# Performance work log

Measured on AMD Instinct MI355X. Metric: run time of the kernel, lower is better.

The kernel has to match this reference:

```python
import jax, jax.numpy as jnp
import numpy as np

HIDDEN = 512
SCALE = 1.0 / np.sqrt(HIDDEN).astype(np.float32)
MASK_FILL = -1e20


def setup_inputs() -> dict:
    key = jax.random.key(0)
    k1, k2 = jax.random.split(key)
    B, S, D = 4, 4096, HIDDEN
    X = jax.random.normal(k1, (B, S, D), dtype=jnp.float32)
    W = jax.random.normal(k2, (D, 3 * D), dtype=jnp.float32) * (1.0 / np.sqrt(D))
    b = jnp.zeros((3 * D,), dtype=jnp.float32)
    attention_mask = jnp.ones((B, 1, S), dtype=jnp.int32)
    return {"X": X, "W": W, "b": b, "attention_mask": attention_mask}


def reference(X, W, b, attention_mask):
    # fused QKV projection: [B,S,3D]
    QKV = jnp.einsum('bsd,de->bse', X, W) + b
    Q, K, V = jnp.split(QKV, 3, axis=-1)
    # full score matrix [B,S,S] (the memory-bound part)
    scores = jnp.einsum('bqd,bkd->bqk', Q, K)
    # faithful: mask BEFORE scaling (fill value also gets divided by sqrt(d))
    scores = jnp.where(attention_mask == 0, MASK_FILL, scores)
    attn = jax.nn.softmax(scores * SCALE, axis=-1)
    # dropout disabled (eval mode) for deterministic reference
    out = jnp.einsum('bqk,bkd->bqd', attn, V)
    return out
```

## Files before the change

kernel.cpp:

```cpp
#include <hip/hip_runtime.h>
#include <cstdint>

#define B_  4
#define S_  4096
#define D_  512

#define SCALEF 0.04419417382415922f
#define QSF    0.06375885f
#define MASK_FILLF -1e20f
#define MASKQ  -6.375885e18f
#define FMAX2  17.312340f

typedef __attribute__((ext_vector_type(8))) short b16x8;
typedef __attribute__((ext_vector_type(4))) float f32x4;
typedef __attribute__((ext_vector_type(16))) float f32x16;

__device__ __forceinline__ unsigned short f2bf(float f) {
    unsigned int u = __builtin_bit_cast(unsigned int, f);
    u += 0x7fffu + ((u >> 16) & 1u);
    return (unsigned short)(u >> 16);
}

__device__ __forceinline__ float exp2fast(float x) {
#if __has_builtin(__builtin_amdgcn_exp2f)
    return __builtin_amdgcn_exp2f(x);
#else
    return __expf(x * 0.69314718056f);
#endif
}

__device__ __forceinline__ void gl_lds16(const void* gp, void* lp) {
    __builtin_amdgcn_global_load_lds(
        (const __attribute__((address_space(1))) unsigned int*)(uintptr_t)gp,
        (__attribute__((address_space(3))) unsigned int*)(uintptr_t)lp,
        16, 0, 0);
}

__global__ __launch_bounds__(256) void cast_x_kernel(const float* __restrict__ X,
                                                     unsigned short* __restrict__ Xb) {
    int i = (blockIdx.x * 256 + threadIdx.x) * 4;
    float4 v = *(const float4*)(X + i);
    ushort4 o;
    o.x = f2bf(v.x); o.y = f2bf(v.y); o.z = f2bf(v.z); o.w = f2bf(v.w);
    *(ushort4*)(Xb + i) = o;
}

__global__ __launch_bounds__(256) void cast_wt_kernel(const float* __restrict__ W,
                                                      unsigned short* __restrict__ Wt) {
    __shared__ float t[32][33];
    int tx = threadIdx.x & 31, ty0 = threadIdx.x >> 5;
    int e0 = blockIdx.x * 32;
    int d0 = blockIdx.y * 32;
#pragma unroll
    for (int p = 0; p < 4; ++p) {
        int ty = ty0 + p * 8;
        t[ty][tx] = W[(size_t)(d0 + ty) * 1536 + e0 + tx];
    }
    __syncthreads();
#pragma unroll
    for (int p = 0; p < 4; ++p) {
        int ty = ty0 + p * 8;
        Wt[(size_t)(e0 + ty) * 512 + d0 + tx] = f2bf(t[tx][ty]);
    }
}

__global__ __launch_bounds__(256) void qkv_gemm_kernel(
    const unsigned short* __restrict__ Xb, const unsigned short* __restrict__ Wt,
    const float* __restrict__ bias,
    unsigned short* __restrict__ Qb, unsigned short* __restrict__ Kb,
    unsigned short* __restrict__ Vt) {
    __shared__ char lds[32768];
    const int tid = threadIdx.x, lane = tid & 63, wave = tid >> 6;
    const int quad = lane >> 4, kcol = lane & 15;
    const int wm = wave & 1, wn = wave >> 1;
    const int row0 = blockIdx.x * 128;
    const int col0 = blockIdx.y * 128;

    unsigned agl[2], bgl[2], lloc[2];
#pragma unroll
    for (int i = 0; i < 2; ++i) {
        int L = (wave * 2 + i) * 64 + lane;
        int r = L >> 2;
        int c = (L & 3) ^ ((r >> 1) & 3);
        agl[i] = (unsigned)((row0 + r) * 1024 + c * 16);
        bgl[i] = (unsigned)((col0 + r) * 1024 + c * 16);
        lloc[i] = (unsigned)(((wave * 2 + i) * 64) * 16);
    }

    f32x4 acc[4][4];
#pragma unroll
    for (int mt = 0; mt < 4; ++mt)
#pragma unroll
        for (int nt = 0; nt < 4; ++nt) acc[mt][nt] = (f32x4){0.f, 0.f, 0.f, 0.f};

    auto stage = [&](int kk) {
        char* la = lds + (kk & 1) * 16384;
        char* lb = la + 8192;
#pragma unroll
        for (int i = 0; i < 2; ++i) {
            gl_lds16((const char*)Xb + agl[i] + kk * 64, la + lloc[i]);
            gl_lds16((const char*)Wt + bgl[i] + kk * 64, lb + lloc[i]);
        }
    };

    stage(0);
    for (int kk = 0; kk < 16; ++kk) {
        __syncthreads();
        if (kk < 15) stage(kk + 1);
        const char* la = lds + (kk & 1) * 16384;
        const char* lb = la + 8192;
        b16x8 af[4], bfr[4];
#pragma unroll
        for (int mt = 0; mt < 4; ++mt) {
            int rr = wm * 64 + mt * 16 + kcol;
            af[mt] = *(const b16x8*)(la + rr * 64 + ((quad ^ ((rr >> 1) & 3)) << 4));
        }
#pragma unroll
        for (int nt = 0; nt < 4; ++nt) {
            int rr = wn * 64 + nt * 16 + kcol;
            bfr[nt] = *(const b16x8*)(lb + rr * 64 + ((quad ^ ((rr >> 1) & 3)) << 4));
        }
#pragma unroll
        for (int mt = 0; mt < 4; ++mt)
#pragma unroll
            for (int nt = 0; nt < 4; ++nt)
                acc[mt][nt] = __builtin_amdgcn_mfma_f32_16x16x32_bf16(af[mt], bfr[nt], acc[mt][nt], 0, 0, 0);
    }

    const int colbase = col0 + wn * 64;
    const int sec = colbase >> 9;
    const int cbase = colbase & 511;
    float bv[4];
#pragma unroll
    for (int nt = 0; nt < 4; ++nt) bv[nt] = bias[colbase + nt * 16 + kcol];

    if (sec < 2) {
        unsigned short* dst = sec == 0 ? Qb : Kb;
        const float scl = sec == 0 ? QSF : 1.0f;
#pragma unroll
        for (int mt = 0; mt < 4; ++mt) {
            int rg0 = row0 + wm * 64 + mt * 16 + quad * 4;
#pragma unroll
            for (int r = 0; r < 4; ++r) {
                size_t rowoff = (size_t)(rg0 + r) * 512;
#pragma unroll
                for (int nt = 0; nt < 4; ++nt)
                    dst[rowoff + cbase + nt * 16 + kcol] = f2bf((acc[mt][nt][r] + bv[nt]) * scl);
            }
        }
    } else {
#pragma unroll
        for (int mt = 0; mt < 4; ++mt) {
            int g0 = row0 + wm * 64 + mt * 16 + quad * 4;
#pragma unroll
            for (int r = 0; r < 4; ++r) {
                int g = g0 + r;
                int s = g & 4095;
                size_t pbase = (((size_t)(g >> 12) * 128 + (s >> 5)) << 14) + (s & 31);
#pragma unroll
                for (int nt = 0; nt < 4; ++nt) {
                    int d = cbase + nt * 16 + kcol;
                    Vt[pbase + (size_t)d * 32] = f2bf(acc[mt][nt][r] + bv[nt]);
                }
            }
        }
    }
}

__global__ __launch_bounds__(384, 2) void flash_kernel(
    const unsigned short* __restrict__ Qb, const unsigned short* __restrict__ Kb,
    const unsigned short* __restrict__ Vt, const int* __restrict__ maskG,
    float* __restrict__ Out) {
    extern __shared__ char smem[];
    const int tid = threadIdx.x;
    const int lane = tid & 63;
    const int wave = tid >> 6;
    const int lin = blockIdx.x;
    const int b = lin & 3;
    const int qrow0 = (lin >> 2) * 64;
    const int NT = 128;

    char* ldsK = smem;
    unsigned short* Pb = (unsigned short*)(smem + 65536);
    float* lbuf = (float*)Pb;

    const char* kgbase = (const char*)(Kb + (size_t)b * S_ * D_);
    const char* vgbase = (const char*)Vt + (size_t)b * 128 * 32768;
    const int* mrow = maskG + b * S_;

    if (wave < 2) {
        const int keyrow = lane & 31;
        const int hh = lane >> 5;
        const int swz = lane & 7;

        b16x8 qf[32];
        {
            const unsigned short* qptr =
                Qb + (size_t)(b * S_ + qrow0 + wave * 32 + keyrow) * D_ + hh * 8;
#pragma unroll
            for (int ks = 0; ks < 32; ++ks) qf[ks] = *(const b16x8*)(qptr + ks * 16);
        }
        float lsum16[16];
#pragma unroll
        for (int r = 0; r < 16; ++r) lsum16[r] = 0.f;

        for (int t = 0; t < NT; ++t) {
            __syncthreads();
            const char* kl = ldsK + (t & 1) * 32768;
            f32x16 sA, sB;
#pragma unroll
            for (int i = 0; i < 16; ++i) { sA[i] = 0.f; sB[i] = 0.f; }
#pragma unroll
            for (int ks = 0; ks < 32; ++ks) {
                b16x8 kf = *(const b16x8*)(kl + keyrow * 1024 +
                                           (((ks * 2 + hh) ^ swz) << 4));
                if (ks & 1) sB = __builtin_amdgcn_mfma_f32_32x32x16_bf16(qf[ks], kf, sB, 0, 0, 0);
                else        sA = __builtin_amdgcn_mfma_f32_32x32x16_bf16(qf[ks], kf, sA, 0, 0, 0);
            }
            const bool um = mrow[t * 32 + keyrow] != 0;
            unsigned short* Pcur = Pb + (t & 1) * 2560;
#pragma unroll
            for (int r = 0; r < 16; ++r) {
                float sv = sA[r] + sB[r];
                float lg = um ? sv : MASKQ;
                float ex = exp2fast(lg - FMAX2);
                lsum16[r] += ex;
                int row = (r & 3) + 8 * (r >> 2) + 4 * hh + wave * 32;
                Pcur[row * 40 + keyrow] = f2bf(ex);
            }
        }
        __syncthreads();

#pragma unroll
        for (int r = 0; r < 16; ++r) {
            float l = lsum16[r];
            l += __shfl_xor(l, 1);
            l += __shfl_xor(l, 2);
            l += __shfl_xor(l, 4);
            l += __shfl_xor(l, 8);
            l += __shfl_xor(l, 16);
            if (keyrow == 0) {
                int row = (r & 3) + 8 * (r >> 2) + 4 * hh + wave * 32;
                lbuf[row] = 1.0f / l;
            }
        }
        __syncthreads();
    } else {
        const int ws = wave - 2;
        const int dw = ws * 128;
        const int quad = lane >> 4;
        const int kcol = lane & 15;

        unsigned kgl[8], kll[8];
#pragma unroll
        for (int i = 0; i < 8; ++i) {
            int r = ws * 8 + i;
            kgl[i] = (unsigned)(r * 1024 + (lane ^ i) * 16);
            kll[i] = (unsigned)(r * 1024);
        }

        f32x4 o[4][8];
#pragma unroll
        for (int m = 0; m < 4; ++m)
#pragma unroll
            for (int n = 0; n < 8; ++n) o[m][n] = (f32x4){0.f, 0.f, 0.f, 0.f};

        {
#pragma unroll
            for (int i = 0; i < 8; ++i) gl_lds16(kgbase + kgl[i], ldsK + kll[i]);
        }

        for (int t = 0; t < NT; ++t) {
            __syncthreads();

            b16x8 vf[8];
            if (t > 0) {
                const char* vtile = vgbase + (size_t)(t - 1) * 32768;
#pragma unroll
                for (int n = 0; n < 8; ++n)
                    vf[n] = *(const b16x8*)(vtile + (size_t)(dw + n * 16 + kcol) * 64 + quad * 16);
            }

            if (t + 1 < NT) {
                const char* kg = kgbase + (size_t)(t + 1) * 32768;
                char* kl2 = ldsK + ((t + 1) & 1) * 32768;
#pragma unroll
                for (int i = 0; i < 8; ++i) gl_lds16(kg + kgl[i], kl2 + kll[i]);
            }

            if (t > 0) {
                const unsigned short* Pprev = Pb + ((t - 1) & 1) * 2560;
#pragma unroll
                for (int m = 0; m < 4; ++m) {
                    b16x8 pf = *(const b16x8*)((const char*)Pprev + (m * 16 + kcol) * 80 + quad * 16);
#pragma unroll
                    for (int n = 0; n < 8; ++n)
                        o[m][n] = __builtin_amdgcn_mfma_f32_16x16x32_bf16(pf, vf[n], o[m][n], 0, 0, 0);
                }
            }
        }
        __syncthreads();

        {
            const char* vtile = vgbase + (size_t)(NT - 1) * 32768;
            b16x8 vf[8];
#pragma unroll
            for (int n = 0; n < 8; ++n)
                vf[n] = *(const b16x8*)(vtile + (size_t)(dw + n * 16 + kcol) * 64 + quad * 16);
            const unsigned short* Pprev = Pb + ((NT - 1) & 1) * 2560;
#pragma unroll
            for (int m = 0; m < 4; ++m) {
                b16x8 pf = *(const b16x8*)((const char*)Pprev + (m * 16 + kcol) * 80 + quad * 16);
#pragma unroll
                for (int n = 0; n < 8; ++n)
                    o[m][n] = __builtin_amdgcn_mfma_f32_16x16x32_bf16(pf, vf[n], o[m][n], 0, 0, 0);
            }
        }
        __syncthreads();

#pragma unroll
        for (int m = 0; m < 4; ++m) {
            f32x4 lv = *(const f32x4*)(lbuf + m * 16 + quad * 4);
#pragma unroll
            for (int r = 0; r < 4; ++r) {
                size_t off = ((size_t)b * S_ + qrow0 + m * 16 + quad * 4 + r) * D_ + dw + kcol;
#pragma unroll
                for (int n = 0; n < 8; ++n) Out[off + n * 16] = o[m][n][r] * lv[r];
            }
        }
    }
}

extern "C" void kernel_launch(void* const* d_in, const int* in_sizes, int n_in,
                              void* d_out, int out_size, void* d_ws, size_t ws_size,
                              hipStream_t stream) {
    const float* X = (const float*)d_in[0];
    const float* W = (const float*)d_in[1];
    const float* bias = (const float*)d_in[2];
    const int* mask = (const int*)d_in[3];
    float* out = (float*)d_out;

    char* w = (char*)d_ws;
    unsigned short* Xb = (unsigned short*)w;  w += (size_t)16384 * 512 * 2;
    unsigned short* Wt = (unsigned short*)w;  w += (size_t)1536 * 512 * 2;
    unsigned short* Qb = (unsigned short*)w;  w += (size_t)16384 * 512 * 2;
    unsigned short* Kb = (unsigned short*)w;  w += (size_t)16384 * 512 * 2;
    unsigned short* Vt = (unsigned short*)w;  w += (size_t)16384 * 512 * 2;

    cast_x_kernel<<<8192, 256, 0, stream>>>(X, Xb);
    cast_wt_kernel<<<dim3(48, 16), 256, 0, stream>>>(W, Wt);
    qkv_gemm_kernel<<<dim3(128, 12), 256, 0, stream>>>(Xb, Wt, bias, Qb, Kb, Vt);

    (void)hipFuncSetAttribute((const void*)flash_kernel,
                              hipFuncAttributeMaxDynamicSharedMemorySize, 75776);
    flash_kernel<<<256, 384, 75776, stream>>>(Qb, Kb, Vt, mask, out);
}
```

Measured before the change: 320.9 us.

## Process two 32-key tiles per pipeline stage to halve barrier count

The flash kernel now stages 64 keys per iteration instead of 32, so the K buffer in LDS is double-buffered at 64 KB per half and two P tiles are produced and consumed per stage. This halves the number of __syncthreads handoffs between the score waves and the PV waves, and gives each wave more MFMA work between barriers. The PV waves now load P fragments into registers up front, and the K swizzle is adjusted for the wider tile. The cost is dynamic LDS growing to about 148 KB, which limits residency to one block per CU.

```diff
diff --git a/kernel.cpp b/kernel.cpp
--- a/kernel.cpp
+++ b/kernel.cpp
@@ -178,10 +178,10 @@
     const int lin = blockIdx.x;
     const int b = lin & 3;
     const int qrow0 = (lin >> 2) * 64;
-    const int NT = 128;
+    const int NI = 64;
 
     char* ldsK = smem;
-    unsigned short* Pb = (unsigned short*)(smem + 65536);
+    unsigned short* Pb = (unsigned short*)(smem + 131072);
     float* lbuf = (float*)Pb;
 
     const char* kgbase = (const char*)(Kb + (size_t)b * S_ * D_);
@@ -204,29 +204,33 @@
 #pragma unroll
         for (int r = 0; r < 16; ++r) lsum16[r] = 0.f;
 
-        for (int t = 0; t < NT; ++t) {
+        for (int it = 0; it < NI; ++it) {
             __syncthreads();
-            const char* kl = ldsK + (t & 1) * 32768;
-            f32x16 sA, sB;
-#pragma unroll
-            for (int i = 0; i < 16; ++i) { sA[i] = 0.f; sB[i] = 0.f; }
-#pragma unroll
-            for (int ks = 0; ks < 32; ++ks) {
-                b16x8 kf = *(const b16x8*)(kl + keyrow * 1024 +
-                                           (((ks * 2 + hh) ^ swz) << 4));
-                if (ks & 1) sB = __builtin_amdgcn_mfma_f32_32x32x16_bf16(qf[ks], kf, sB, 0, 0, 0);
-                else        sA = __builtin_amdgcn_mfma_f32_32x32x16_bf16(qf[ks], kf, sA, 0, 0, 0);
-            }
-            const bool um = mrow[t * 32 + keyrow] != 0;
-            unsigned short* Pcur = Pb + (t & 1) * 2560;
-#pragma unroll
-            for (int r = 0; r < 16; ++r) {
-                float sv = sA[r] + sB[r];
-                float lg = um ? sv : MASKQ;
-                float ex = exp2fast(lg - FMAX2);
-                lsum16[r] += ex;
-                int row = (r & 3) + 8 * (r >> 2) + 4 * hh + wave * 32;
-                Pcur[row * 40 + keyrow] = f2bf(ex);
+            const char* kl = ldsK + (it & 1) * 65536;
+            unsigned short* Ppar = Pb + (it & 1) * 5120;
+#pragma unroll
+            for (int h = 0; h < 2; ++h) {
+                const bool um = mrow[it * 64 + h * 32 + keyrow] != 0;
+                f32x16 sA, sB;
+#pragma unroll
+                for (int i = 0; i < 16; ++i) { sA[i] = 0.f; sB[i] = 0.f; }
+#pragma unroll
+                for (int ks = 0; ks < 32; ++ks) {
+                    b16x8 kf = *(const b16x8*)(kl + (h * 32 + keyrow) * 1024 +
+                                               (((ks * 2 + hh) ^ swz) << 4));
+                    if (ks & 1) sB = __builtin_amdgcn_mfma_f32_32x32x16_bf16(qf[ks], kf, sB, 0, 0, 0);
+                    else        sA = __builtin_amdgcn_mfma_f32_32x32x16_bf16(qf[ks], kf, sA, 0, 0, 0);
+                }
+                unsigned short* Pcur = Ppar + h * 2560;
+#pragma unroll
+                for (int r = 0; r < 16; ++r) {
+                    float sv = sA[r] + sB[r];
+                    float lg = um ? sv : MASKQ;
+                    float ex = exp2fast(lg - FMAX2);
+                    lsum16[r] += ex;
+                    int row = (r & 3) + 8 * (r >> 2) + 4 * hh + wave * 32;
+                    Pcur[row * 40 + keyrow] = f2bf(ex);
+                }
             }
         }
         __syncthreads();
@@ -239,7 +243,7 @@
             l += __shfl_xor(l, 4);
             l += __shfl_xor(l, 8);
             l += __shfl_xor(l, 16);
-            if (keyrow == 0) {
+            if ((lane & 31) == 0) {
                 int row = (r & 3) + 8 * (r >> 2) + 4 * hh + wave * 32;
                 lbuf[row] = 1.0f / l;
             }
@@ -251,11 +255,11 @@
         const int quad = lane >> 4;
         const int kcol = lane & 15;
 
-        unsigned kgl[8], kll[8];
-#pragma unroll
-        for (int i = 0; i < 8; ++i) {
-            int r = ws * 8 + i;
-            kgl[i] = (unsigned)(r * 1024 + (lane ^ i) * 16);
+        unsigned kgl[16], kll[16];
+#pragma unroll
+        for (int i = 0; i < 16; ++i) {
+            int r = ws * 16 + i;
+            kgl[i] = (unsigned)(r * 1024 + (lane ^ (r & 7)) * 16);
             kll[i] = (unsigned)(r * 1024);
         }
 
@@ -267,53 +271,73 @@
 
         {
 #pragma unroll
-            for (int i = 0; i < 8; ++i) gl_lds16(kgbase + kgl[i], ldsK + kll[i]);
-        }
-
-        for (int t = 0; t < NT; ++t) {
+            for (int i = 0; i < 16; ++i) gl_lds16(kgbase + kgl[i], ldsK + kll[i]);
+        }
+
+        for (int it = 0; it < NI; ++it) {
             __syncthreads();
 
-            b16x8 vf[8];
-            if (t > 0) {
-                const char* vtile = vgbase + (size_t)(t - 1) * 32768;
+            b16x8 vf[8], pf[4];
+            const unsigned short* Ppar = Pb + ((it ^ 1) & 1) * 5120;
+            if (it > 0) {
+                const char* vtile = vgbase + (size_t)((it - 1) * 2) * 32768;
 #pragma unroll
                 for (int n = 0; n < 8; ++n)
                     vf[n] = *(const b16x8*)(vtile + (size_t)(dw + n * 16 + kcol) * 64 + quad * 16);
-            }
-
-            if (t + 1 < NT) {
-                const char* kg = kgbase + (size_t)(t + 1) * 32768;
-                char* kl2 = ldsK + ((t + 1) & 1) * 32768;
-#pragma unroll
-                for (int i = 0; i < 8; ++i) gl_lds16(kg + kgl[i], kl2 + kll[i]);
-            }
-
-            if (t > 0) {
-                const unsigned short* Pprev = Pb + ((t - 1) & 1) * 2560;
-#pragma unroll
-                for (int m = 0; m < 4; ++m) {
-                    b16x8 pf = *(const b16x8*)((const char*)Pprev + (m * 16 + kcol) * 80 + quad * 16);
+#pragma unroll
+                for (int m = 0; m < 4; ++m)
+                    pf[m] = *(const b16x8*)((const char*)Ppar + (m * 16 + kcol) * 80 + quad * 16);
+            }
+
+            if (it + 1 < NI) {
+                const char* kg = kgbase + (size_t)(it + 1) * 65536;
+                char* kl2 = ldsK + ((it + 1) & 1) * 65536;
+#pragma unroll
+                for (int i = 0; i < 16; ++i) gl_lds16(kg + kgl[i], kl2 + kll[i]);
+            }
+
+            if (it > 0) {
+#pragma unroll
+                for (int m = 0; m < 4; ++m)
 #pragma unroll
                     for (int n = 0; n < 8; ++n)
-                        o[m][n] = __builtin_amdgcn_mfma_f32_16x16x32_bf16(pf, vf[n], o[m][n], 0, 0, 0);
-                }
+                        o[m][n] = __builtin_amdgcn_mfma_f32_16x16x32_bf16(pf[m], vf[n], o[m][n], 0, 0, 0);
+
+                const char* vtileb = vgbase + (size_t)((it - 1) * 2 + 1) * 32768;
+#pragma unroll
+                for (int n = 0; n < 8; ++n)
+                    vf[n] = *(const b16x8*)(vtileb + (size_t)(dw + n * 16 + kcol) * 64 + quad * 16);
+                const unsigned short* Pcb = Ppar + 2560;
+#pragma unroll
+                for (int m = 0; m < 4; ++m)
+                    pf[m] = *(const b16x8*)((const char*)Pcb + (m * 16 + kcol) * 80 + quad * 16);
+#pragma unroll
+                for (int m = 0; m < 4; ++m)
+#pragma unroll
+                    for (int n = 0; n < 8; ++n)
+                        o[m][n] = __builtin_amdgcn_mfma_f32_16x16x32_bf16(pf[m], vf[n], o[m][n], 0, 0, 0);
             }
         }
         __syncthreads();
 
         {
-            const char* vtile = vgbase + (size_t)(NT - 1) * 32768;
-            b16x8 vf[8];
-#pragma unroll
-            for (int n = 0; n < 8; ++n)
-                vf[n] = *(const b16x8*)(vtile + (size_t)(dw + n * 16 + kcol) * 64 + quad * 16);
-            const unsigned short* Pprev = Pb + ((NT - 1) & 1) * 2560;
-#pragma unroll
-            for (int m = 0; m < 4; ++m) {
-                b16x8 pf = *(const b16x8*)((const char*)Pprev + (m * 16 + kcol) * 80 + quad * 16);
+            const unsigned short* Ppar = Pb + ((NI - 1) & 1) * 5120;
+#pragma unroll
+            for (int h = 0; h < 2; ++h) {
+                const char* vtile = vgbase + (size_t)((NI - 1) * 2 + h) * 32768;
+                b16x8 vf[8], pf[4];
 #pragma unroll
                 for (int n = 0; n < 8; ++n)
-                    o[m][n] = __builtin_amdgcn_mfma_f32_16x16x32_bf16(pf, vf[n], o[m][n], 0, 0, 0);
+                    vf[n] = *(const b16x8*)(vtile + (size_t)(dw + n * 16 + kcol) * 64 + quad * 16);
+                const unsigned short* Pcur = Ppar + h * 2560;
+#pragma unroll
+                for (int m = 0; m < 4; ++m)
+                    pf[m] = *(const b16x8*)((const char*)Pcur + (m * 16 + kcol) * 80 + quad * 16);
+#pragma unroll
+                for (int m = 0; m < 4; ++m)
+#pragma unroll
+                    for (int n = 0; n < 8; ++n)
+                        o[m][n] = __builtin_amdgcn_mfma_f32_16x16x32_bf16(pf[m], vf[n], o[m][n], 0, 0, 0);
             }
         }
         __syncthreads();
@@ -352,6 +376,6 @@
     qkv_gemm_kernel<<<dim3(128, 12), 256, 0, stream>>>(Xb, Wt, bias, Qb, Kb, Vt);
 
     (void)hipFuncSetAttribute((const void*)flash_kernel,
-                              hipFuncAttributeMaxDynamicSharedMemorySize, 75776);
-    flash_kernel<<<256, 384, 75776, stream>>>(Qb, Kb, Vt, mask, out);
-}
+                              hipFuncAttributeMaxDynamicSharedMemorySize, 151552);
+    flash_kernel<<<256, 384, 151552, stream>>>(Qb, Kb, Vt, mask, out);
+}
```

Measured after the change: 311.8 us. 2.8% less time.
